# Optimization experiments

Hardware: AMD Instinct MI355X
Metric: run time of the kernel (lower is better)

The kernel has to match this reference:

```python
import jax, jax.numpy as jnp
import numpy as np

NUM_UNITS = 32   # nodes per graph (obs_dim 160 / 5)
B = 2048         # graphs per batch
FEAT_IN = 5
NUM_OUT = 5


def setup_inputs() -> dict:
    key = jax.random.key(0)
    ks = jax.random.split(key, 16)
    obs = jax.random.normal(ks[0], (B, NUM_UNITS * FEAT_IN), dtype=jnp.float32)
    # Fully-connected (incl. self-loop) edge list per graph, offset by graph id.
    i = jnp.arange(NUM_UNITS, dtype=jnp.int32)
    s, d = jnp.meshgrid(i, i, indexing='ij')          # all 32x32 pairs
    offs = (jnp.arange(B, dtype=jnp.int32) * NUM_UNITS)[:, None]
    src = (s.reshape(-1)[None, :] + offs).reshape(-1)  # [B*1024]
    dst = (d.reshape(-1)[None, :] + offs).reshape(-1)
    def lin(k, fin, fout):
        return jax.random.normal(k, (fout, fin), dtype=jnp.float32) * (1.0 / np.sqrt(fin))
    return {
        'obs': obs, 'src': src, 'dst': dst,
        'W1l': lin(ks[1], 5, 64),  'b1': jnp.zeros((64,), jnp.float32),  'W1r': lin(ks[2], 5, 64),
        'W2l': lin(ks[3], 64, 128), 'b2': jnp.zeros((128,), jnp.float32), 'W2r': lin(ks[4], 64, 128),
        'W3l': lin(ks[5], 128, 128), 'b3': jnp.zeros((128,), jnp.float32), 'W3r': lin(ks[6], 128, 128),
        'Wp': lin(ks[7], 128, NUM_OUT), 'bp': jnp.zeros((NUM_OUT,), jnp.float32),
    }


def reference(obs, src, dst, W1l, b1, W1r, W2l, b2, W2r, W3l, b3, W3r, Wp, bp):
    x = obs.reshape(-1, FEAT_IN)                 # [N, 5], N = B*32
    N = x.shape[0]
    deg = jnp.float32(NUM_UNITS)                 # every node has 32 in-edges

    def sage(h, Wl, b, Wr):
        # PyG SAGEConv: lin_l(mean_{j->i} h_j) + lin_r(h_i); bias lives in lin_l
        msg = h[src]                             # gather  [E, F]
        agg = jax.ops.segment_sum(msg, dst, num_segments=N) / deg
        return agg @ Wl.T + b + h @ Wr.T

    h = jax.nn.relu(sage(x, W1l, b1, W1r))
    h = jax.nn.relu(sage(h, W2l, b2, W2r))
    h = jax.nn.relu(sage(h, W3l, b3, W3r))
    pooled = h.reshape(B, NUM_UNITS, 128).mean(axis=1)   # global_mean_pool (equal-size graphs)
    return pooled @ Wp.T + bp                    # policy_out [B, NUM_OUT]
```

## Files before the change

kernel.cpp:

```cpp
#include <hip/hip_runtime.h>
#include <hip/hip_bf16.h>


typedef float f32x4 __attribute__((ext_vector_type(4)));
typedef __bf16 bf16x8 __attribute__((ext_vector_type(8)));
typedef unsigned short u16x4 __attribute__((ext_vector_type(4)));

__device__ __forceinline__ f32x4 MFMA(bf16x8 a, bf16x8 b, f32x4 c) {
  return __builtin_amdgcn_mfma_f32_16x16x32_bf16(a, b, c, 0, 0, 0);
}

__device__ __forceinline__ unsigned short bfbits(float v) {
  __hip_bfloat16 t = __float2bfloat16(v);
  return __builtin_bit_cast(unsigned short, t);
}

__device__ __forceinline__ u16x4 pack4(f32x4 v) {
  u16x4 r;
  r[0] = bfbits(v[0]); r[1] = bfbits(v[1]);
  r[2] = bfbits(v[2]); r[3] = bfbits(v[3]);
  return r;
}

__device__ __forceinline__ bf16x8 pack8(f32x4 lo, f32x4 hi) {
  union { bf16x8 v; unsigned short u[8]; } t;
  t.u[0] = bfbits(lo[0]); t.u[1] = bfbits(lo[1]);
  t.u[2] = bfbits(lo[2]); t.u[3] = bfbits(lo[3]);
  t.u[4] = bfbits(hi[0]); t.u[5] = bfbits(hi[1]);
  t.u[6] = bfbits(hi[2]); t.u[7] = bfbits(hi[3]);
  return t.v;
}

__global__ __launch_bounds__(256) void gnn_prep(
    const float* __restrict__ W1l, const float* __restrict__ W1r,
    const float* __restrict__ W2l, const float* __restrict__ W2r,
    const float* __restrict__ W3l, const float* __restrict__ W3r,
    unsigned short* __restrict__ wpack)
{
  int e = blockIdx.x * 256 + threadIdx.x;
  if (e >= 53248) return;
  const float* src; int Kreal, KS, eloc;
  if      (e < 2048)  { src = W1r; Kreal = 5;   KS = 1; eloc = e; }
  else if (e < 4096)  { src = W1l; Kreal = 5;   KS = 1; eloc = e - 2048; }
  else if (e < 12288) { src = W2r; Kreal = 64;  KS = 2; eloc = e - 4096; }
  else if (e < 20480) { src = W2l; Kreal = 64;  KS = 2; eloc = e - 12288; }
  else if (e < 36864) { src = W3r; Kreal = 128; KS = 4; eloc = e - 20480; }
  else                { src = W3l; Kreal = 128; KS = 4; eloc = e - 36864; }
  int j = eloc & 7, lane = (eloc >> 3) & 63, rest = eloc >> 9;
  int ks = rest % KS, ft = rest / KS;
  int f = ft * 16 + (lane & 15);
  int k = ks * 32 + (lane >> 4) * 8 + j;
  float v = (k < Kreal) ? src[f * Kreal + k] : 0.f;
  wpack[e] = bfbits(v);
}

#define RBW 136

__global__ __launch_bounds__(512) void gnn_fused(
    const float* __restrict__ obs,
    const float* __restrict__ b1, const float* __restrict__ b2,
    const float* __restrict__ b3,
    const float* __restrict__ Wp, const float* __restrict__ bp,
    const unsigned short* __restrict__ wpack,
    float* __restrict__ out)
{
  __shared__ unsigned short smW[32768];
  __shared__ unsigned short rb_all[8][32 * RBW];
  __shared__ unsigned short mb_all[8][128];
  __shared__ float mbf_all[8][128];

  const int tid  = threadIdx.x;
  const int wid  = tid >> 6;
  const int lane = tid & 63;
  const int g    = lane >> 4;
  const int c    = lane & 15;
  unsigned short* rbb = &rb_all[wid][0];
  unsigned short* mbb = &mb_all[wid][0];
  float* mbf = &mbf_all[wid][0];
  const int graph = blockIdx.x * 8 + wid;
  const float* xg = obs + graph * 160;

  const unsigned short* A1r = wpack;
  const unsigned short* A1l = wpack + 2048;
  const unsigned short* A2r = wpack + 4096;
  const unsigned short* A2l = wpack + 12288;

  {
    const unsigned short* gA3 = wpack + 20480;
#pragma unroll
    for (int it = 0; it < 8; ++it) {
      const int chunk = it * 8 + wid;
      const void* gsrc = (const void*)((const char*)(gA3 + chunk * 512) + lane * 16);
      __builtin_amdgcn_global_load_lds(
          (const __attribute__((address_space(1))) unsigned int*)gsrc,
          (__attribute__((address_space(3))) unsigned int*)&smW[chunk * 512],
          16, 0, 0);
    }
  }

  const f32x4 Z4 = {0.f, 0.f, 0.f, 0.f};

  float x0[5], x1[5];
#pragma unroll
  for (int j = 0; j < 5; ++j) { x0[j] = xg[c * 5 + j]; x1[j] = xg[80 + c * 5 + j]; }
  float m0[5];
#pragma unroll
  for (int j = 0; j < 5; ++j) {
    float s = x0[j] + x1[j];
    s += __shfl_xor(s, 1, 64); s += __shfl_xor(s, 2, 64);
    s += __shfl_xor(s, 4, 64); s += __shfl_xor(s, 8, 64);
    m0[j] = s * 0.03125f;
  }
  bf16x8 Bn1[2], Bg1;
  {
    f32x4 a0 = {x0[0], x0[1], x0[2], x0[3]}, a1 = {x0[4], 0.f, 0.f, 0.f};
    f32x4 n0 = {x1[0], x1[1], x1[2], x1[3]}, n1 = {x1[4], 0.f, 0.f, 0.f};
    f32x4 g0 = {m0[0], m0[1], m0[2], m0[3]}, g1 = {m0[4], 0.f, 0.f, 0.f};
    if (g != 0) { a0 = Z4; a1 = Z4; n0 = Z4; n1 = Z4; g0 = Z4; g1 = Z4; }
    Bn1[0] = pack8(a0, a1); Bn1[1] = pack8(n0, n1); Bg1 = pack8(g0, g1);
  }

  f32x4 acc[2][8];
#pragma unroll
  for (int ft = 0; ft < 4; ++ft) {
    f32x4 bias = *(const f32x4*)(b1 + ft * 16 + 4 * g);
    acc[0][ft] = bias; acc[1][ft] = bias;
    bf16x8 ar = *(const bf16x8*)(A1r + (ft * 64 + lane) * 8);
    bf16x8 al = *(const bf16x8*)(A1l + (ft * 64 + lane) * 8);
    acc[0][ft] = MFMA(ar, Bn1[0], acc[0][ft]);
    acc[1][ft] = MFMA(ar, Bn1[1], acc[1][ft]);
    acc[0][ft] = MFMA(al, Bg1, acc[0][ft]);
    acc[1][ft] = MFMA(al, Bg1, acc[1][ft]);
  }
#pragma unroll
  for (int ct = 0; ct < 2; ++ct)
#pragma unroll
    for (int ft = 0; ft < 4; ++ft)
#pragma unroll
      for (int i = 0; i < 4; ++i)
        acc[ct][ft][i] = fmaxf(acc[ct][ft][i], 0.f);

#pragma unroll
  for (int ft = 0; ft < 4; ++ft) {
    *(u16x4*)(rbb + c * RBW        + ft * 16 + 4 * g) = pack4(acc[0][ft]);
    *(u16x4*)(rbb + (16 + c) * RBW + ft * 16 + 4 * g) = pack4(acc[1][ft]);
    f32x4 s = acc[0][ft] + acc[1][ft];
#pragma unroll
    for (int i = 0; i < 4; ++i) {
      float v = s[i];
      v += __shfl_xor(v, 1, 64); v += __shfl_xor(v, 2, 64);
      v += __shfl_xor(v, 4, 64); v += __shfl_xor(v, 8, 64);
      s[i] = v * 0.03125f;
    }
    if (c == 0) *(u16x4*)(mbb + ft * 16 + 4 * g) = pack4(s);
  }

  bf16x8 Bn[2][4], Bg[4];
#pragma unroll
  for (int ct = 0; ct < 2; ++ct)
#pragma unroll
    for (int ks = 0; ks < 2; ++ks)
      Bn[ct][ks] = *(const bf16x8*)(rbb + (ct * 16 + c) * RBW + 32 * ks + 8 * g);
#pragma unroll
  for (int ks = 0; ks < 2; ++ks)
    Bg[ks] = *(const bf16x8*)(mbb + 32 * ks + 8 * g);

#pragma unroll
  for (int ft = 0; ft < 8; ++ft) {
    f32x4 bias = *(const f32x4*)(b2 + ft * 16 + 4 * g);
    acc[0][ft] = bias; acc[1][ft] = bias;
#pragma unroll
    for (int ks = 0; ks < 2; ++ks) {
      bf16x8 ar = *(const bf16x8*)(A2r + ((ft * 2 + ks) * 64 + lane) * 8);
      bf16x8 al = *(const bf16x8*)(A2l + ((ft * 2 + ks) * 64 + lane) * 8);
      acc[0][ft] = MFMA(ar, Bn[0][ks], acc[0][ft]);
      acc[1][ft] = MFMA(ar, Bn[1][ks], acc[1][ft]);
      acc[0][ft] = MFMA(al, Bg[ks], acc[0][ft]);
      acc[1][ft] = MFMA(al, Bg[ks], acc[1][ft]);
    }
  }
#pragma unroll
  for (int ct = 0; ct < 2; ++ct)
#pragma unroll
    for (int ft = 0; ft < 8; ++ft)
#pragma unroll
      for (int i = 0; i < 4; ++i)
        acc[ct][ft][i] = fmaxf(acc[ct][ft][i], 0.f);

#pragma unroll
  for (int ft = 0; ft < 8; ++ft) {
    *(u16x4*)(rbb + c * RBW        + ft * 16 + 4 * g) = pack4(acc[0][ft]);
    *(u16x4*)(rbb + (16 + c) * RBW + ft * 16 + 4 * g) = pack4(acc[1][ft]);
    f32x4 s = acc[0][ft] + acc[1][ft];
#pragma unroll
    for (int i = 0; i < 4; ++i) {
      float v = s[i];
      v += __shfl_xor(v, 1, 64); v += __shfl_xor(v, 2, 64);
      v += __shfl_xor(v, 4, 64); v += __shfl_xor(v, 8, 64);
      s[i] = v * 0.03125f;
    }
    if (c == 0) *(u16x4*)(mbb + ft * 16 + 4 * g) = pack4(s);
  }

#pragma unroll
  for (int ct = 0; ct < 2; ++ct)
#pragma unroll
    for (int ks = 0; ks < 4; ++ks)
      Bn[ct][ks] = *(const bf16x8*)(rbb + (ct * 16 + c) * RBW + 32 * ks + 8 * g);
#pragma unroll
  for (int ks = 0; ks < 4; ++ks)
    Bg[ks] = *(const bf16x8*)(mbb + 32 * ks + 8 * g);

  asm volatile("s_waitcnt vmcnt(0)" ::: "memory");
  __syncthreads();

  {
    const unsigned short* A3r = smW;
    const unsigned short* A3l = smW + 16384;
#pragma unroll
    for (int ft = 0; ft < 8; ++ft) {
      f32x4 bias = *(const f32x4*)(b3 + ft * 16 + 4 * g);
      acc[0][ft] = bias; acc[1][ft] = bias;
#pragma unroll
      for (int ks = 0; ks < 4; ++ks) {
        bf16x8 ar = *(const bf16x8*)(A3r + ((ft * 4 + ks) * 64 + lane) * 8);
        bf16x8 al = *(const bf16x8*)(A3l + ((ft * 4 + ks) * 64 + lane) * 8);
        acc[0][ft] = MFMA(ar, Bn[0][ks], acc[0][ft]);
        acc[1][ft] = MFMA(ar, Bn[1][ks], acc[1][ft]);
        acc[0][ft] = MFMA(al, Bg[ks], acc[0][ft]);
        acc[1][ft] = MFMA(al, Bg[ks], acc[1][ft]);
      }
    }
  }
#pragma unroll
  for (int ct = 0; ct < 2; ++ct)
#pragma unroll
    for (int ft = 0; ft < 8; ++ft)
#pragma unroll
      for (int i = 0; i < 4; ++i)
        acc[ct][ft][i] = fmaxf(acc[ct][ft][i], 0.f);

#pragma unroll
  for (int ft = 0; ft < 8; ++ft) {
    f32x4 s = acc[0][ft] + acc[1][ft];
#pragma unroll
    for (int i = 0; i < 4; ++i) {
      float v = s[i];
      v += __shfl_xor(v, 1, 64); v += __shfl_xor(v, 2, 64);
      v += __shfl_xor(v, 4, 64); v += __shfl_xor(v, 8, 64);
      s[i] = v * 0.03125f;
    }
    if (c == 0) *(f32x4*)(mbf + ft * 16 + 4 * g) = s;
  }

  float p0 = mbf[lane], p1 = mbf[64 + lane];
  float po[5];
#pragma unroll
  for (int o = 0; o < 5; ++o)
    po[o] = p0 * Wp[o * 128 + lane] + p1 * Wp[o * 128 + 64 + lane];
#pragma unroll
  for (int o = 0; o < 5; ++o) {
    float v = po[o];
    v += __shfl_xor(v, 1, 64);  v += __shfl_xor(v, 2, 64);
    v += __shfl_xor(v, 4, 64);  v += __shfl_xor(v, 8, 64);
    v += __shfl_xor(v, 16, 64); v += __shfl_xor(v, 32, 64);
    po[o] = v;
  }
  if (lane == 0) {
#pragma unroll
    for (int o = 0; o < 5; ++o) out[graph * 5 + o] = po[o] + bp[o];
  }
}

extern "C" void kernel_launch(void* const* d_in, const int* in_sizes, int n_in,
                              void* d_out, int out_size, void* d_ws, size_t ws_size,
                              hipStream_t stream)
{
  const float* obs = (const float*)d_in[0];
  const float* W1l = (const float*)d_in[3];
  const float* b1  = (const float*)d_in[4];
  const float* W1r = (const float*)d_in[5];
  const float* W2l = (const float*)d_in[6];
  const float* b2  = (const float*)d_in[7];
  const float* W2r = (const float*)d_in[8];
  const float* W3l = (const float*)d_in[9];
  const float* b3  = (const float*)d_in[10];
  const float* W3r = (const float*)d_in[11];
  const float* Wp  = (const float*)d_in[12];
  const float* bp  = (const float*)d_in[13];
  unsigned short* wpack = (unsigned short*)d_ws;
  float* out = (float*)d_out;

  gnn_prep<<<208, 256, 0, stream>>>(W1l, W1r, W2l, W2r, W3l, W3r, wpack);
  gnn_fused<<<256, 512, 0, stream>>>(obs, b1, b2, b3, Wp, bp, wpack, out);
}
```

Measured before the change: 26.86 us.

## Fuse weight packing into main kernel, converting fp32 weights to bf16 in-kernel

Removes the separate weight-prep kernel launch. The main kernel now reads fp32 weights directly: layer-1 weights go into registers, layer-2 weights are loaded and packed per MFMA, and each block converts layer-3 weights into a padded row-major bf16 LDS tile. This drops one launch and the workspace round-trip. In exchange, every block redoes the conversion, reads twice as many bytes for W2/W3, and the layer-3 loads become synchronous global loads instead of async global-to-LDS copies.

```diff
diff --git a/kernel.cpp b/kernel.cpp
--- a/kernel.cpp
+++ b/kernel.cpp
@@ -31,40 +31,20 @@
   return t.v;
 }
 
-__global__ __launch_bounds__(256) void gnn_prep(
+#define RBW 136
+#define W3ROWS 256
+
+__global__ __launch_bounds__(512) void gnn_all(
+    const float* __restrict__ obs,
     const float* __restrict__ W1l, const float* __restrict__ W1r,
     const float* __restrict__ W2l, const float* __restrict__ W2r,
     const float* __restrict__ W3l, const float* __restrict__ W3r,
-    unsigned short* __restrict__ wpack)
-{
-  int e = blockIdx.x * 256 + threadIdx.x;
-  if (e >= 53248) return;
-  const float* src; int Kreal, KS, eloc;
-  if      (e < 2048)  { src = W1r; Kreal = 5;   KS = 1; eloc = e; }
-  else if (e < 4096)  { src = W1l; Kreal = 5;   KS = 1; eloc = e - 2048; }
-  else if (e < 12288) { src = W2r; Kreal = 64;  KS = 2; eloc = e - 4096; }
-  else if (e < 20480) { src = W2l; Kreal = 64;  KS = 2; eloc = e - 12288; }
-  else if (e < 36864) { src = W3r; Kreal = 128; KS = 4; eloc = e - 20480; }
-  else                { src = W3l; Kreal = 128; KS = 4; eloc = e - 36864; }
-  int j = eloc & 7, lane = (eloc >> 3) & 63, rest = eloc >> 9;
-  int ks = rest % KS, ft = rest / KS;
-  int f = ft * 16 + (lane & 15);
-  int k = ks * 32 + (lane >> 4) * 8 + j;
-  float v = (k < Kreal) ? src[f * Kreal + k] : 0.f;
-  wpack[e] = bfbits(v);
-}
-
-#define RBW 136
-
-__global__ __launch_bounds__(512) void gnn_fused(
-    const float* __restrict__ obs,
     const float* __restrict__ b1, const float* __restrict__ b2,
     const float* __restrict__ b3,
     const float* __restrict__ Wp, const float* __restrict__ bp,
-    const unsigned short* __restrict__ wpack,
     float* __restrict__ out)
 {
-  __shared__ unsigned short smW[32768];
+  __shared__ unsigned short smw3[W3ROWS * RBW];
   __shared__ unsigned short rb_all[8][32 * RBW];
   __shared__ unsigned short mb_all[8][128];
   __shared__ float mbf_all[8][128];
@@ -80,29 +60,43 @@
   const int graph = blockIdx.x * 8 + wid;
   const float* xg = obs + graph * 160;
 
-  const unsigned short* A1r = wpack;
-  const unsigned short* A1l = wpack + 2048;
-  const unsigned short* A2r = wpack + 4096;
-  const unsigned short* A2l = wpack + 12288;
+  float x0[5], x1[5];
+#pragma unroll
+  for (int j = 0; j < 5; ++j) { x0[j] = xg[c * 5 + j]; x1[j] = xg[80 + c * 5 + j]; }
+
+  bf16x8 ar1[4], al1[4];
+#pragma unroll
+  for (int ft = 0; ft < 4; ++ft) {
+    float wr[8] = {0,0,0,0,0,0,0,0}, wl[8] = {0,0,0,0,0,0,0,0};
+    if (g == 0) {
+#pragma unroll
+      for (int j = 0; j < 5; ++j) {
+        wr[j] = W1r[(ft * 16 + c) * 5 + j];
+        wl[j] = W1l[(ft * 16 + c) * 5 + j];
+      }
+    }
+    f32x4 rlo = {wr[0], wr[1], wr[2], wr[3]}, rhi = {wr[4], 0.f, 0.f, 0.f};
+    f32x4 llo = {wl[0], wl[1], wl[2], wl[3]}, lhi = {wl[4], 0.f, 0.f, 0.f};
+    ar1[ft] = pack8(rlo, rhi);
+    al1[ft] = pack8(llo, lhi);
+  }
 
   {
-    const unsigned short* gA3 = wpack + 20480;
-#pragma unroll
-    for (int it = 0; it < 8; ++it) {
-      const int chunk = it * 8 + wid;
-      const void* gsrc = (const void*)((const char*)(gA3 + chunk * 512) + lane * 16);
-      __builtin_amdgcn_global_load_lds(
-          (const __attribute__((address_space(1))) unsigned int*)gsrc,
-          (__attribute__((address_space(3))) unsigned int*)&smW[chunk * 512],
-          16, 0, 0);
+    const int row  = tid >> 1;
+    const int half = tid & 1;
+    const float* src = ((row < 128) ? (W3r + row * 128)
+                                    : (W3l + (row - 128) * 128)) + half * 64;
+    unsigned short* dst = smw3 + row * RBW + half * 64;
+#pragma unroll
+    for (int i = 0; i < 8; ++i) {
+      f32x4 lo = *(const f32x4*)(src + i * 8);
+      f32x4 hi = *(const f32x4*)(src + i * 8 + 4);
+      *(bf16x8*)(dst + i * 8) = pack8(lo, hi);
     }
   }
 
   const f32x4 Z4 = {0.f, 0.f, 0.f, 0.f};
 
-  float x0[5], x1[5];
-#pragma unroll
-  for (int j = 0; j < 5; ++j) { x0[j] = xg[c * 5 + j]; x1[j] = xg[80 + c * 5 + j]; }
   float m0[5];
 #pragma unroll
   for (int j = 0; j < 5; ++j) {
@@ -125,12 +119,10 @@
   for (int ft = 0; ft < 4; ++ft) {
     f32x4 bias = *(const f32x4*)(b1 + ft * 16 + 4 * g);
     acc[0][ft] = bias; acc[1][ft] = bias;
-    bf16x8 ar = *(const bf16x8*)(A1r + (ft * 64 + lane) * 8);
-    bf16x8 al = *(const bf16x8*)(A1l + (ft * 64 + lane) * 8);
-    acc[0][ft] = MFMA(ar, Bn1[0], acc[0][ft]);
-    acc[1][ft] = MFMA(ar, Bn1[1], acc[1][ft]);
-    acc[0][ft] = MFMA(al, Bg1, acc[0][ft]);
-    acc[1][ft] = MFMA(al, Bg1, acc[1][ft]);
+    acc[0][ft] = MFMA(ar1[ft], Bn1[0], acc[0][ft]);
+    acc[1][ft] = MFMA(ar1[ft], Bn1[1], acc[1][ft]);
+    acc[0][ft] = MFMA(al1[ft], Bg1, acc[0][ft]);
+    acc[1][ft] = MFMA(al1[ft], Bg1, acc[1][ft]);
   }
 #pragma unroll
   for (int ct = 0; ct < 2; ++ct)
@@ -171,8 +163,10 @@
     acc[0][ft] = bias; acc[1][ft] = bias;
 #pragma unroll
     for (int ks = 0; ks < 2; ++ks) {
-      bf16x8 ar = *(const bf16x8*)(A2r + ((ft * 2 + ks) * 64 + lane) * 8);
-      bf16x8 al = *(const bf16x8*)(A2l + ((ft * 2 + ks) * 64 + lane) * 8);
+      const float* pr = W2r + (ft * 16 + c) * 64 + ks * 32 + 8 * g;
+      const float* pl = W2l + (ft * 16 + c) * 64 + ks * 32 + 8 * g;
+      bf16x8 ar = pack8(*(const f32x4*)pr, *(const f32x4*)(pr + 4));
+      bf16x8 al = pack8(*(const f32x4*)pl, *(const f32x4*)(pl + 4));
       acc[0][ft] = MFMA(ar, Bn[0][ks], acc[0][ft]);
       acc[1][ft] = MFMA(ar, Bn[1][ks], acc[1][ft]);
       acc[0][ft] = MFMA(al, Bg[ks], acc[0][ft]);
@@ -202,29 +196,28 @@
     if (c == 0) *(u16x4*)(mbb + ft * 16 + 4 * g) = pack4(s);
   }
 
-#pragma unroll
-  for (int ct = 0; ct < 2; ++ct)
+  __syncthreads();
+
+  {
+    const unsigned short* A3r = smw3;
+    const unsigned short* A3l = smw3 + 128 * RBW;
+#pragma unroll
+    for (int ct = 0; ct < 2; ++ct)
+#pragma unroll
+      for (int ks = 0; ks < 4; ++ks)
+        Bn[ct][ks] = *(const bf16x8*)(rbb + (ct * 16 + c) * RBW + 32 * ks + 8 * g);
 #pragma unroll
     for (int ks = 0; ks < 4; ++ks)
-      Bn[ct][ks] = *(const bf16x8*)(rbb + (ct * 16 + c) * RBW + 32 * ks + 8 * g);
-#pragma unroll
-  for (int ks = 0; ks < 4; ++ks)
-    Bg[ks] = *(const bf16x8*)(mbb + 32 * ks + 8 * g);
-
-  asm volatile("s_waitcnt vmcnt(0)" ::: "memory");
-  __syncthreads();
-
-  {
-    const unsigned short* A3r = smW;
-    const unsigned short* A3l = smW + 16384;
+      Bg[ks] = *(const bf16x8*)(mbb + 32 * ks + 8 * g);
+
 #pragma unroll
     for (int ft = 0; ft < 8; ++ft) {
       f32x4 bias = *(const f32x4*)(b3 + ft * 16 + 4 * g);
       acc[0][ft] = bias; acc[1][ft] = bias;
 #pragma unroll
       for (int ks = 0; ks < 4; ++ks) {
-        bf16x8 ar = *(const bf16x8*)(A3r + ((ft * 4 + ks) * 64 + lane) * 8);
-        bf16x8 al = *(const bf16x8*)(A3l + ((ft * 4 + ks) * 64 + lane) * 8);
+        bf16x8 ar = *(const bf16x8*)(A3r + (ft * 16 + c) * RBW + ks * 32 + 8 * g);
+        bf16x8 al = *(const bf16x8*)(A3l + (ft * 16 + c) * RBW + ks * 32 + 8 * g);
         acc[0][ft] = MFMA(ar, Bn[0][ks], acc[0][ft]);
         acc[1][ft] = MFMA(ar, Bn[1][ks], acc[1][ft]);
         acc[0][ft] = MFMA(al, Bg[ks], acc[0][ft]);
@@ -288,9 +281,8 @@
   const float* W3r = (const float*)d_in[11];
   const float* Wp  = (const float*)d_in[12];
   const float* bp  = (const float*)d_in[13];
-  unsigned short* wpack = (unsigned short*)d_ws;
   float* out = (float*)d_out;
 
-  gnn_prep<<<208, 256, 0, stream>>>(W1l, W1r, W2l, W2r, W3l, W3r, wpack);
-  gnn_fused<<<256, 512, 0, stream>>>(obs, b1, b2, b3, Wp, bp, wpack, out);
-}
+  gnn_all<<<256, 512, 0, stream>>>(obs, W1l, W1r, W2l, W2r, W3l, W3r,
+                                   b1, b2, b3, Wp, bp, out);
+}
```

New measurement: 34.06 us. 1.27x slower.
